# Kernel optimization log

Hardware: AMD Instinct MI355X
Metric: run time of the kernel (lower is better)

## Reference

```python
import jax, jax.numpy as jnp
import numpy as np

N = 100000
E = 1600000
F_IN, H, C = 128, 128, 64


def setup_inputs() -> dict:
    key = jax.random.key(0)
    ks = jax.random.split(key, 8)
    x = jax.random.normal(ks[0], (N, F_IN), dtype=jnp.float32)
    edge_index = jax.random.randint(ks[1], (2, E), 0, N, dtype=jnp.int64)
    s = lambda fi: (1.0 / np.sqrt(fi))
    # SAGEConv1: lin_l (applied to mean-aggregated neighbors, has bias), lin_r (root, no bias)
    W1l = jax.random.uniform(ks[2], (H, F_IN), jnp.float32, -s(F_IN), s(F_IN))
    b1 = jnp.zeros((H,), jnp.float32)
    W1r = jax.random.uniform(ks[3], (H, F_IN), jnp.float32, -s(F_IN), s(F_IN))
    # SAGEConv2
    W2l = jax.random.uniform(ks[4], (C, H), jnp.float32, -s(H), s(H))
    b2 = jnp.zeros((C,), jnp.float32)
    W2r = jax.random.uniform(ks[5], (C, H), jnp.float32, -s(H), s(H))
    return {"x": x, "edge_index": edge_index, "W1l": W1l, "b1": b1, "W1r": W1r,
            "W2l": W2l, "b2": b2, "W2r": W2r}


def _mean_aggr(x, src, dst):
    # mean over incoming neighbors (PyG flow: edge_index[0]=source -> edge_index[1]=target)
    msg = x[src]                                            # [E, F] big gather
    summed = jax.ops.segment_sum(msg, dst, num_segments=N)  # [N, F]
    cnt = jax.ops.segment_sum(jnp.ones((src.shape[0],), x.dtype), dst, num_segments=N)
    return summed / jnp.clip(cnt, 1.0)[:, None]


def _sage_conv(x, src, dst, Wl, b, Wr):
    agg = _mean_aggr(x, src, dst)
    return agg @ Wl.T + b + x @ Wr.T


def _iconv(x, src, dst):
    # weight-free GCN propagation: D^-1/2 (A + I) D^-1/2 @ x
    loops = jnp.arange(N, dtype=src.dtype)
    s2 = jnp.concatenate([src, loops])
    d2 = jnp.concatenate([dst, loops])
    deg = jax.ops.segment_sum(jnp.ones((s2.shape[0],), x.dtype), d2, num_segments=N)
    dis = jnp.where(deg > 0, jax.lax.rsqrt(jnp.maximum(deg, 1.0)), 0.0)
    norm = dis[s2] * dis[d2]                               # [E+N]
    return jax.ops.segment_sum(norm[:, None] * x[s2], d2, num_segments=N)


def reference(x, edge_index, W1l, b1, W1r, W2l, b2, W2r):
    src, dst = edge_index[0], edge_index[1]
    h = jax.nn.relu(_sage_conv(x, src, dst, W1l, b1, W1r))
    # F.dropout(training=False) -> identity in eval mode
    h = _sage_conv(h, src, dst, W2l, b2, W2r)
    return _iconv(h, src, dst)
```

## Files before the change

### kernel.cpp

```cpp
#include <hip/hip_runtime.h>

#define GN 100000
#define GE 1600000
#define GF 128
#define GH 128
#define GC 64

#define NB 392
#define SLABSZ 5376
#define P1_EDGES 4096
#define P1_BLOCKS ((GE + P1_EDGES - 1) / P1_EDGES)
#define CASTX_BLOCKS 12500

typedef __attribute__((ext_vector_type(8))) short v8s;
typedef __attribute__((ext_vector_type(4))) float v4f;
typedef __attribute__((ext_vector_type(2))) float v2f;

__device__ __forceinline__ unsigned short f2bf(float f) {
    union { float f; unsigned u; } a; a.f = f;
    unsigned r = a.u + 0x7fff + ((a.u >> 16) & 1);
    return (unsigned short)(r >> 16);
}
__device__ __forceinline__ float bf2f(unsigned short b) {
    union { unsigned u; float f; } a; a.u = ((unsigned)b) << 16;
    return a.f;
}
__device__ __forceinline__ v2f cvt2(unsigned w) {
    union { unsigned u; float f; } lo, hi;
    lo.u = w << 16; hi.u = w & 0xffff0000u;
    return (v2f){lo.f, hi.f};
}

__global__ __launch_bounds__(256) void prep_kernel(
    unsigned* __restrict__ slab, int* __restrict__ bucket_cnt,
    const int* __restrict__ src, const int* __restrict__ dst,
    unsigned short* __restrict__ xb, const float* __restrict__ x,
    unsigned short* w1l, unsigned short* w1r,
    unsigned short* w2l, unsigned short* w2r,
    const float* W1l, const float* W1r,
    const float* W2l, const float* W2r)
{
    __shared__ int hist[512];
    __shared__ int scanex[512];
    __shared__ int cursor[512];
    __shared__ int gbase[512];
    __shared__ int ssum[256];
    __shared__ unsigned stage[P1_EDGES];
    __shared__ unsigned short sbid[P1_EDGES];

    int tid = threadIdx.x;
    int blk = blockIdx.x;

    if (blk >= P1_BLOCKS) {
        int cb = blk - P1_BLOCKS;
        if (cb < CASTX_BLOCKS) {
            int i = cb * 256 + tid;
            float4 v = ((const float4*)x)[i];
            ushort4 u;
            u.x = f2bf(v.x); u.y = f2bf(v.y); u.z = f2bf(v.z); u.w = f2bf(v.w);
            ((ushort4*)xb)[i] = u;
            return;
        }
        int i = (cb - CASTX_BLOCKS) * 256 + tid;
        const float* s; unsigned short* d; int off;
        if      (i <  4096) { s = W1l; d = w1l; off = i; }
        else if (i <  8192) { s = W1r; d = w1r; off = i - 4096; }
        else if (i < 10240) { s = W2l; d = w2l; off = i - 8192; }
        else if (i < 12288) { s = W2r; d = w2r; off = i - 10240; }
        else return;
        float4 v = ((const float4*)s)[off];
        ushort4 u;
        u.x = f2bf(v.x); u.y = f2bf(v.y); u.z = f2bf(v.z); u.w = f2bf(v.w);
        ((ushort4*)d)[off] = u;
        return;
    }

    int e0 = blk * P1_EDGES;
    int nE = min(P1_EDGES, GE - e0);

    unsigned pk[16]; int bk[16];
    hist[tid] = 0; hist[tid + 256] = 0;
    __syncthreads();
    #pragma unroll
    for (int j = 0; j < 16; ++j) {
        int i = j * 256 + tid;
        if (i < nE) {
            int e = e0 + i;
            int d = dst[e], s = src[e];
            int b = d >> 8;
            pk[j] = ((unsigned)(d & 255) << 17) | (unsigned)s;
            bk[j] = b;
            atomicAdd(&hist[b], 1);
        } else bk[j] = -1;
    }
    __syncthreads();
    int a0 = hist[2 * tid], a1 = hist[2 * tid + 1];
    int s2 = a0 + a1;
    ssum[tid] = s2;
    __syncthreads();
    for (int off = 1; off < 256; off <<= 1) {
        int v = (tid >= off) ? ssum[tid - off] : 0;
        __syncthreads();
        ssum[tid] += v;
        __syncthreads();
    }
    int pbase = ssum[tid] - s2;
    scanex[2 * tid] = pbase;          cursor[2 * tid] = pbase;
    scanex[2 * tid + 1] = pbase + a0; cursor[2 * tid + 1] = pbase + a0;
    __syncthreads();
    #pragma unroll
    for (int j = 0; j < 16; ++j) {
        if (bk[j] >= 0) {
            int pos = atomicAdd(&cursor[bk[j]], 1);
            stage[pos] = pk[j];
            sbid[pos] = (unsigned short)bk[j];
        }
    }
    for (int b = tid; b < NB; b += 256) {
        int c = hist[b];
        gbase[b] = c ? atomicAdd(&bucket_cnt[b], c) : 0;
    }
    __syncthreads();
    for (int i = tid; i < nE; i += 256) {
        int b = sbid[i];
        int go = gbase[b] + (i - scanex[b]);
        if (go < SLABSZ)
            slab[(size_t)b * SLABSZ + go] = stage[i];
    }
}

__global__ __launch_bounds__(256) void bucket_pass2_kernel(
    int* __restrict__ csr, int* __restrict__ row_ptr,
    float* __restrict__ invc, float* __restrict__ dis,
    const unsigned* __restrict__ slab, const int* __restrict__ bucket_cnt)
{
    __shared__ int deg_l[256];
    __shared__ int excl[256];
    __shared__ int cur[256];
    __shared__ int ssum[256];
    __shared__ int bstart_s;
    __shared__ unsigned stage[SLABSZ];

    int t = threadIdx.x;
    int b = blockIdx.x;

    int c0 = (2 * t < NB) ? bucket_cnt[2 * t] : 0;
    int c1 = (2 * t + 1 < NB) ? bucket_cnt[2 * t + 1] : 0;
    int sc = c0 + c1;
    ssum[t] = sc;
    __syncthreads();
    for (int off = 1; off < 256; off <<= 1) {
        int v = (t >= off) ? ssum[t - off] : 0;
        __syncthreads();
        ssum[t] += v;
        __syncthreads();
    }
    int pb = ssum[t] - sc;
    if (2 * t == b)     bstart_s = pb;
    if (2 * t + 1 == b) bstart_s = pb + c0;
    if (b == NB - 1 && t == 0) row_ptr[GN] = GE;

    int cnt = min(bucket_cnt[b], SLABSZ);
    const unsigned* sp = slab + (size_t)b * SLABSZ;
    deg_l[t] = 0;
    __syncthreads();
    int base = bstart_s;
    for (int i = t; i < cnt; i += 256)
        atomicAdd(&deg_l[sp[i] >> 17], 1);
    __syncthreads();
    int dg = deg_l[t];
    ssum[t] = dg;
    __syncthreads();
    for (int off = 1; off < 256; off <<= 1) {
        int v = (t >= off) ? ssum[t - off] : 0;
        __syncthreads();
        ssum[t] += v;
        __syncthreads();
    }
    int ex = ssum[t] - dg;
    excl[t] = ex; cur[t] = ex;
    __syncthreads();
    int d = b * 256 + t;
    if (d < GN) {
        row_ptr[d] = base + ex;
        float c = (float)dg;
        invc[d] = 1.0f / fmaxf(c, 1.0f);
        dis[d] = rsqrtf(c + 1.0f);
    }
    for (int i = t; i < cnt; i += 256) {
        unsigned p = sp[i];
        int pos = atomicAdd(&cur[p >> 17], 1);
        stage[pos] = p & 0x1FFFFu;
    }
    __syncthreads();
    for (int i = t; i < cnt; i += 256)
        csr[base + i] = (int)stage[i];
}

__global__ __launch_bounds__(64, 2) void fused_gemm_kernel(
    unsigned short* __restrict__ P, unsigned short* __restrict__ Q,
    const unsigned short* __restrict__ A1, const unsigned short* __restrict__ A2,
    const unsigned short* __restrict__ W1, const unsigned short* __restrict__ W2,
    const unsigned short* __restrict__ Wl, const unsigned short* __restrict__ Wr,
    const float* __restrict__ b1, const float* __restrict__ b2, int M)
{
    __shared__ unsigned short hs[64][136];

    int lane = threadIdx.x;
    int lm = lane & 15, quad = lane >> 4;
    int m_base = blockIdx.x * 64;

    v4f acc[4][8];
    #pragma unroll
    for (int mt = 0; mt < 4; ++mt)
        #pragma unroll
        for (int nt = 0; nt < 8; ++nt) acc[mt][nt] = (v4f){0.f,0.f,0.f,0.f};

    #pragma unroll
    for (int ks = 0; ks < 4; ++ks) {
        int koff = ks * 32 + quad * 8;
        v8s a1[4], a2[4];
        #pragma unroll
        for (int mt = 0; mt < 4; ++mt) {
            int row = m_base + mt * 16 + lm;
            if (row < M) {
                a1[mt] = *(const v8s*)(A1 + (size_t)row * 128 + koff);
                a2[mt] = *(const v8s*)(A2 + (size_t)row * 128 + koff);
            } else {
                a1[mt] = (v8s){0,0,0,0,0,0,0,0};
                a2[mt] = (v8s){0,0,0,0,0,0,0,0};
            }
        }
        v8s w1[8], w2[8];
        #pragma unroll
        for (int nt = 0; nt < 8; ++nt) {
            int col = nt * 16 + lm;
            w1[nt] = *(const v8s*)(W1 + (size_t)col * 128 + koff);
            w2[nt] = *(const v8s*)(W2 + (size_t)col * 128 + koff);
        }
        #pragma unroll
        for (int mt = 0; mt < 4; ++mt)
            #pragma unroll
            for (int nt = 0; nt < 8; ++nt) {
                acc[mt][nt] = __builtin_amdgcn_mfma_f32_16x16x32_bf16(a1[mt], w1[nt], acc[mt][nt], 0, 0, 0);
                acc[mt][nt] = __builtin_amdgcn_mfma_f32_16x16x32_bf16(a2[mt], w2[nt], acc[mt][nt], 0, 0, 0);
            }
    }

    #pragma unroll
    for (int mt = 0; mt < 4; ++mt)
        #pragma unroll
        for (int r = 0; r < 4; ++r) {
            int rl = mt * 16 + quad * 4 + r;
            #pragma unroll
            for (int nt = 0; nt < 8; ++nt) {
                int col = nt * 16 + lm;
                float v = acc[mt][nt][r] + b1[col];
                hs[rl][col] = f2bf(fmaxf(v, 0.f));
            }
        }

    v4f accP[4][4], accQ[4][4];
    #pragma unroll
    for (int mt = 0; mt < 4; ++mt)
        #pragma unroll
        for (int nt = 0; nt < 4; ++nt) {
            accP[mt][nt] = (v4f){0.f,0.f,0.f,0.f};
            accQ[mt][nt] = (v4f){0.f,0.f,0.f,0.f};
        }

    #pragma unroll
    for (int ks = 0; ks < 4; ++ks) {
        int koff = ks * 32 + quad * 8;
        v8s af[4], bl[4], br[4];
        #pragma unroll
        for (int mt = 0; mt < 4; ++mt)
            af[mt] = *(const v8s*)&hs[mt * 16 + lm][koff];
        #pragma unroll
        for (int nt = 0; nt < 4; ++nt) {
            int col = nt * 16 + lm;
            bl[nt] = *(const v8s*)(Wl + (size_t)col * 128 + koff);
            br[nt] = *(const v8s*)(Wr + (size_t)col * 128 + koff);
        }
        #pragma unroll
        for (int mt = 0; mt < 4; ++mt)
            #pragma unroll
            for (int nt = 0; nt < 4; ++nt) {
                accP[mt][nt] = __builtin_amdgcn_mfma_f32_16x16x32_bf16(af[mt], bl[nt], accP[mt][nt], 0, 0, 0);
                accQ[mt][nt] = __builtin_amdgcn_mfma_f32_16x16x32_bf16(af[mt], br[nt], accQ[mt][nt], 0, 0, 0);
            }
    }

    #pragma unroll
    for (int mt = 0; mt < 4; ++mt)
        #pragma unroll
        for (int r = 0; r < 4; ++r) {
            int row = m_base + mt * 16 + quad * 4 + r;
            if (row >= M) continue;
            #pragma unroll
            for (int nt = 0; nt < 4; ++nt) {
                int col = nt * 16 + lm;
                P[(size_t)row * 64 + col] = f2bf(accP[mt][nt][r]);
                Q[(size_t)row * 64 + col] = f2bf(accQ[mt][nt][r] + b2[col]);
            }
        }
}

__global__ __launch_bounds__(256) void gather_mean128_kernel(
    unsigned short* __restrict__ out, const unsigned short* __restrict__ in,
    const float* __restrict__ invc, const int* __restrict__ row_ptr,
    const int* __restrict__ csr, int N)
{
    int wid = (blockIdx.x * 256 + threadIdx.x) >> 6;
    int lane = threadIdx.x & 63;
    if (wid >= N) return;
    int beg = __builtin_amdgcn_readfirstlane(row_ptr[wid]);
    int end = __builtin_amdgcn_readfirstlane(row_ptr[wid + 1]);
    int d = end - beg;
    int grp = lane >> 4, lx = lane & 15;
    v2f a0 = {0.f,0.f}, a1 = {0.f,0.f}, a2 = {0.f,0.f}, a3 = {0.f,0.f};

    int nf = d >> 2;
    #pragma unroll 4
    for (int t = 0; t < nf; ++t) {
        int j = beg + t * 4;
        int s0 = csr[j], s1 = csr[j + 1], s2 = csr[j + 2], s3 = csr[j + 3];
        int sa = (lane & 16) ? s1 : s0;
        int sb = (lane & 16) ? s3 : s2;
        int ss = (lane & 32) ? sb : sa;
        uint4 v = ((const uint4*)(in + (size_t)ss * 128))[lx];
        a0 += cvt2(v.x); a1 += cvt2(v.y); a2 += cvt2(v.z); a3 += cvt2(v.w);
    }
    int rem = d & 3;
    if (rem) {
        int j = beg + nf * 4;
        int c1 = (rem > 1) ? 1 : 0;
        int c2 = (rem > 2) ? 2 : c1;
        int s0 = csr[j], s1 = csr[j + c1], s2 = csr[j + c2], s3 = s2;
        int sa = (lane & 16) ? s1 : s0;
        int sb = (lane & 16) ? s3 : s2;
        int ss = (lane & 32) ? sb : sa;
        uint4 v = ((const uint4*)(in + (size_t)ss * 128))[lx];
        bool ok = grp < rem;
        v.x = ok ? v.x : 0u; v.y = ok ? v.y : 0u;
        v.z = ok ? v.z : 0u; v.w = ok ? v.w : 0u;
        a0 += cvt2(v.x); a1 += cvt2(v.y); a2 += cvt2(v.z); a3 += cvt2(v.w);
    }
    a0.x += __shfl_xor(a0.x, 16); a0.y += __shfl_xor(a0.y, 16);
    a1.x += __shfl_xor(a1.x, 16); a1.y += __shfl_xor(a1.y, 16);
    a2.x += __shfl_xor(a2.x, 16); a2.y += __shfl_xor(a2.y, 16);
    a3.x += __shfl_xor(a3.x, 16); a3.y += __shfl_xor(a3.y, 16);
    a0.x += __shfl_xor(a0.x, 32); a0.y += __shfl_xor(a0.y, 32);
    a1.x += __shfl_xor(a1.x, 32); a1.y += __shfl_xor(a1.y, 32);
    a2.x += __shfl_xor(a2.x, 32); a2.y += __shfl_xor(a2.y, 32);
    a3.x += __shfl_xor(a3.x, 32); a3.y += __shfl_xor(a3.y, 32);
    if (grp == 0) {
        float ic = invc[wid];
        uint4 o;
        o.x = (unsigned)f2bf(a0.x * ic) | ((unsigned)f2bf(a0.y * ic) << 16);
        o.y = (unsigned)f2bf(a1.x * ic) | ((unsigned)f2bf(a1.y * ic) << 16);
        o.z = (unsigned)f2bf(a2.x * ic) | ((unsigned)f2bf(a2.y * ic) << 16);
        o.w = (unsigned)f2bf(a3.x * ic) | ((unsigned)f2bf(a3.y * ic) << 16);
        ((uint4*)(out + (size_t)wid * 128))[lx] = o;
    }
}

__global__ __launch_bounds__(256) void gather_combine_kernel(
    unsigned short* __restrict__ h2s, const unsigned short* __restrict__ p,
    const unsigned short* __restrict__ q,
    const float* __restrict__ invc, const float* __restrict__ dis,
    const int* __restrict__ row_ptr, const int* __restrict__ csr, int N)
{
    int wid = (blockIdx.x * 256 + threadIdx.x) >> 6;
    int lane = threadIdx.x & 63;
    if (wid >= N) return;
    int beg = __builtin_amdgcn_readfirstlane(row_ptr[wid]);
    int end = __builtin_amdgcn_readfirstlane(row_ptr[wid + 1]);
    int d = end - beg;
    int grp = lane >> 3, lx = lane & 7;
    v2f a0 = {0.f,0.f}, a1 = {0.f,0.f}, a2 = {0.f,0.f}, a3 = {0.f,0.f};

    int nf = d >> 3;
    #pragma unroll 2
    for (int t = 0; t < nf; ++t) {
        int j = beg + t * 8;
        int s0 = csr[j],     s1 = csr[j + 1], s2 = csr[j + 2], s3 = csr[j + 3];
        int s4 = csr[j + 4], s5 = csr[j + 5], s6 = csr[j + 6], s7 = csr[j + 7];
        int t0 = (lane & 8) ? s1 : s0; int t1 = (lane & 8) ? s3 : s2;
        int t2 = (lane & 8) ? s5 : s4; int t3 = (lane & 8) ? s7 : s6;
        int u0 = (lane & 16) ? t1 : t0; int u1 = (lane & 16) ? t3 : t2;
        int ss = (lane & 32) ? u1 : u0;
        uint4 v = ((const uint4*)(p + (size_t)ss * 64))[lx];
        a0 += cvt2(v.x); a1 += cvt2(v.y); a2 += cvt2(v.z); a3 += cvt2(v.w);
    }
    int rem = d & 7;
    if (rem) {
        int j = beg + nf * 8;
        int rc = rem - 1;
        int s0 = csr[j];
        int s1 = csr[j + min(1, rc)]; int s2 = csr[j + min(2, rc)];
        int s3 = csr[j + min(3, rc)]; int s4 = csr[j + min(4, rc)];
        int s5 = csr[j + min(5, rc)]; int s6 = csr[j + min(6, rc)];
        int s7 = csr[j + min(7, rc)];
        int t0 = (lane & 8) ? s1 : s0; int t1 = (lane & 8) ? s3 : s2;
        int t2 = (lane & 8) ? s5 : s4; int t3 = (lane & 8) ? s7 : s6;
        int u0 = (lane & 16) ? t1 : t0; int u1 = (lane & 16) ? t3 : t2;
        int ss = (lane & 32) ? u1 : u0;
        uint4 v = ((const uint4*)(p + (size_t)ss * 64))[lx];
        bool ok = grp < rem;
        v.x = ok ? v.x : 0u; v.y = ok ? v.y : 0u;
        v.z = ok ? v.z : 0u; v.w = ok ? v.w : 0u;
        a0 += cvt2(v.x); a1 += cvt2(v.y); a2 += cvt2(v.z); a3 += cvt2(v.w);
    }
    #pragma unroll
    for (int m = 8; m <= 32; m <<= 1) {
        a0.x += __shfl_xor(a0.x, m); a0.y += __shfl_xor(a0.y, m);
        a1.x += __shfl_xor(a1.x, m); a1.y += __shfl_xor(a1.y, m);
        a2.x += __shfl_xor(a2.x, m); a2.y += __shfl_xor(a2.y, m);
        a3.x += __shfl_xor(a3.x, m); a3.y += __shfl_xor(a3.y, m);
    }
    if (grp == 0) {
        float ic = invc[wid], dd = dis[wid];
        uint4 qv = ((const uint4*)(q + (size_t)wid * 64))[lx];
        v2f q0 = cvt2(qv.x), q1 = cvt2(qv.y), q2 = cvt2(qv.z), q3 = cvt2(qv.w);
        uint4 o;
        o.x = (unsigned)f2bf(dd * (a0.x * ic + q0.x)) | ((unsigned)f2bf(dd * (a0.y * ic + q0.y)) << 16);
        o.y = (unsigned)f2bf(dd * (a1.x * ic + q1.x)) | ((unsigned)f2bf(dd * (a1.y * ic + q1.y)) << 16);
        o.z = (unsigned)f2bf(dd * (a2.x * ic + q2.x)) | ((unsigned)f2bf(dd * (a2.y * ic + q2.y)) << 16);
        o.w = (unsigned)f2bf(dd * (a3.x * ic + q3.x)) | ((unsigned)f2bf(dd * (a3.y * ic + q3.y)) << 16);
        ((uint4*)(h2s + (size_t)wid * 64))[lx] = o;
    }
}

__global__ __launch_bounds__(256) void iconv_kernel(
    float* __restrict__ out, const unsigned short* __restrict__ h2s,
    const float* __restrict__ dis, const int* __restrict__ row_ptr,
    const int* __restrict__ csr, int N)
{
    int wid = (blockIdx.x * 256 + threadIdx.x) >> 6;
    int lane = threadIdx.x & 63;
    if (wid >= N) return;
    int beg = __builtin_amdgcn_readfirstlane(row_ptr[wid]);
    int end = __builtin_amdgcn_readfirstlane(row_ptr[wid + 1]);
    int d = end - beg;
    int grp = lane >> 3, lx = lane & 7;
    v2f a0 = {0.f,0.f}, a1 = {0.f,0.f}, a2 = {0.f,0.f}, a3 = {0.f,0.f};

    int nf = d >> 3;
    #pragma unroll 2
    for (int t = 0; t < nf; ++t) {
        int j = beg + t * 8;
        int s0 = csr[j],     s1 = csr[j + 1], s2 = csr[j + 2], s3 = csr[j + 3];
        int s4 = csr[j + 4], s5 = csr[j + 5], s6 = csr[j + 6], s7 = csr[j + 7];
        int t0 = (lane & 8) ? s1 : s0; int t1 = (lane & 8) ? s3 : s2;
        int t2 = (lane & 8) ? s5 : s4; int t3 = (lane & 8) ? s7 : s6;
        int u0 = (lane & 16) ? t1 : t0; int u1 = (lane & 16) ? t3 : t2;
        int ss = (lane & 32) ? u1 : u0;
        uint4 v = ((const uint4*)(h2s + (size_t)ss * 64))[lx];
        a0 += cvt2(v.x); a1 += cvt2(v.y); a2 += cvt2(v.z); a3 += cvt2(v.w);
    }
    int rem = d & 7;
    if (rem) {
        int j = beg + nf * 8;
        int rc = rem - 1;
        int s0 = csr[j];
        int s1 = csr[j + min(1, rc)]; int s2 = csr[j + min(2, rc)];
        int s3 = csr[j + min(3, rc)]; int s4 = csr[j + min(4, rc)];
        int s5 = csr[j + min(5, rc)]; int s6 = csr[j + min(6, rc)];
        int s7 = csr[j + min(7, rc)];
        int t0 = (lane & 8) ? s1 : s0; int t1 = (lane & 8) ? s3 : s2;
        int t2 = (lane & 8) ? s5 : s4; int t3 = (lane & 8) ? s7 : s6;
        int u0 = (lane & 16) ? t1 : t0; int u1 = (lane & 16) ? t3 : t2;
        int ss = (lane & 32) ? u1 : u0;
        uint4 v = ((const uint4*)(h2s + (size_t)ss * 64))[lx];
        bool ok = grp < rem;
        v.x = ok ? v.x : 0u; v.y = ok ? v.y : 0u;
        v.z = ok ? v.z : 0u; v.w = ok ? v.w : 0u;
        a0 += cvt2(v.x); a1 += cvt2(v.y); a2 += cvt2(v.z); a3 += cvt2(v.w);
    }
    #pragma unroll
    for (int m = 8; m <= 32; m <<= 1) {
        a0.x += __shfl_xor(a0.x, m); a0.y += __shfl_xor(a0.y, m);
        a1.x += __shfl_xor(a1.x, m); a1.y += __shfl_xor(a1.y, m);
        a2.x += __shfl_xor(a2.x, m); a2.y += __shfl_xor(a2.y, m);
        a3.x += __shfl_xor(a3.x, m); a3.y += __shfl_xor(a3.y, m);
    }
    if (grp == 0) {
        uint4 sv = ((const uint4*)(h2s + (size_t)wid * 64))[lx];
        v2f s0 = cvt2(sv.x), s1 = cvt2(sv.y), s2 = cvt2(sv.z), s3 = cvt2(sv.w);
        float dd = dis[wid];
        float4 o0 = make_float4(dd * (a0.x + s0.x), dd * (a0.y + s0.y),
                                dd * (a1.x + s1.x), dd * (a1.y + s1.y));
        float4 o1 = make_float4(dd * (a2.x + s2.x), dd * (a2.y + s2.y),
                                dd * (a3.x + s3.x), dd * (a3.y + s3.y));
        ((float4*)(out + (size_t)wid * 64))[lx * 2]     = o0;
        ((float4*)(out + (size_t)wid * 64))[lx * 2 + 1] = o1;
    }
}

extern "C" void kernel_launch(void* const* d_in, const int* in_sizes, int n_in,
                              void* d_out, int out_size, void* d_ws, size_t ws_size,
                              hipStream_t stream) {
    const float* x   = (const float*)d_in[0];
    const int*   ei  = (const int*)d_in[1];
    const float* W1l = (const float*)d_in[2];
    const float* b1  = (const float*)d_in[3];
    const float* W1r = (const float*)d_in[4];
    const float* W2l = (const float*)d_in[5];
    const float* b2  = (const float*)d_in[6];
    const float* W2r = (const float*)d_in[7];
    float* out = (float*)d_out;

    const int* src = ei;
    const int* dst = ei + GE;

    float* invc = (float*)d_ws;
    float* dis  = invc + GN;
    unsigned short* regA = (unsigned short*)(dis + GN);
    unsigned short* regB = regA + (size_t)GN * 128;
    unsigned short* xb    = regA;
    unsigned short* aggx  = regB;
    unsigned short* w1lb = regB + (size_t)GN * 128;
    unsigned short* w1rb = w1lb + GH * GF;
    unsigned short* w2lb = w1rb + GH * GF;
    unsigned short* w2rb = w2lb + GC * GH;
    int* row_ptr      = (int*)(w2rb + GC * GH);
    int* bucket_cnt   = row_ptr + GN + 1;
    unsigned* slab    = (unsigned*)(bucket_cnt + NB);
    int* csr          = (int*)(slab + (size_t)NB * SLABSZ);
    unsigned short* pq = (unsigned short*)(csr + GE);
    unsigned short* pb = pq;
    unsigned short* qb = pq + (size_t)GN * 64;
    unsigned short* h2s = regB;

    const int T = 256;
    const int g_wave = (GN * 64 + T - 1) / T;
    dim3 g_fused((GN + 63) / 64, 1);

    hipMemsetAsync(bucket_cnt, 0, NB * sizeof(int), stream);
    prep_kernel<<<P1_BLOCKS + CASTX_BLOCKS + 48, T, 0, stream>>>(
        slab, bucket_cnt, src, dst,
        xb, x, w1lb, w1rb, w2lb, w2rb, W1l, W1r, W2l, W2r);

    bucket_pass2_kernel<<<NB, T, 0, stream>>>(csr, row_ptr, invc, dis,
                                              slab, bucket_cnt);

    gather_mean128_kernel<<<g_wave, T, 0, stream>>>(aggx, xb, invc, row_ptr, csr, GN);

    fused_gemm_kernel<<<g_fused, 64, 0, stream>>>(pb, qb, aggx, xb,
                                                  w1lb, w1rb, w2lb, w2rb,
                                                  b1, b2, GN);

    gather_combine_kernel<<<g_wave, T, 0, stream>>>(h2s, pb, qb, invc, dis,
                                                    row_ptr, csr, GN);

    iconv_kernel<<<g_wave, T, 0, stream>>>(out, h2s, dis, row_ptr, csr, GN);
}
```

Measured before the change: 335.2 us.

## Fuse first-layer neighbor mean gather into the SAGE GEMM kernel

Removes the separate gather_mean128 kernel and its bf16 aggregate buffer round-trip. Each 64-thread block now handles 16 nodes: it gathers neighbor rows into shared memory one node at a time, then runs both MFMA GEMM stages on that 16-row tile. This avoids writing and re-reading the 100000x128 aggregate and one kernel launch. In exchange the gather becomes serial per node within a single wave, which gives less memory-level parallelism. The weights are also reloaded from global memory for every 16-row tile instead of every 64 rows.

```diff
diff --git a/kernel.cpp b/kernel.cpp
--- a/kernel.cpp
+++ b/kernel.cpp
@@ -197,171 +197,121 @@
         csr[base + i] = (int)stage[i];
 }
 
-__global__ __launch_bounds__(64, 2) void fused_gemm_kernel(
+__global__ __launch_bounds__(64, 3) void sage1_fused_kernel(
     unsigned short* __restrict__ P, unsigned short* __restrict__ Q,
-    const unsigned short* __restrict__ A1, const unsigned short* __restrict__ A2,
+    const unsigned short* __restrict__ xb,
     const unsigned short* __restrict__ W1, const unsigned short* __restrict__ W2,
     const unsigned short* __restrict__ Wl, const unsigned short* __restrict__ Wr,
-    const float* __restrict__ b1, const float* __restrict__ b2, int M)
+    const float* __restrict__ b1, const float* __restrict__ b2,
+    const float* __restrict__ invc, const int* __restrict__ row_ptr,
+    const int* __restrict__ csr)
 {
-    __shared__ unsigned short hs[64][136];
+    __shared__ unsigned short hsA[16][136];
+    __shared__ unsigned short hsB[16][136];
 
     int lane = threadIdx.x;
     int lm = lane & 15, quad = lane >> 4;
-    int m_base = blockIdx.x * 64;
-
-    v4f acc[4][8];
-    #pragma unroll
-    for (int mt = 0; mt < 4; ++mt)
-        #pragma unroll
-        for (int nt = 0; nt < 8; ++nt) acc[mt][nt] = (v4f){0.f,0.f,0.f,0.f};
+    int m_base = blockIdx.x * 16;
+
+    int rp = row_ptr[m_base + min(lane, 16)];
+    float icv = invc[m_base + lm];
+
+    for (int r = 0; r < 16; ++r) {
+        int beg = __builtin_amdgcn_readlane(rp, r);
+        int end = __builtin_amdgcn_readlane(rp, r + 1);
+        int d = end - beg;
+        float a0 = 0.f, a1 = 0.f;
+        if (d > 0) {
+            int dc = min(d, 64);
+            int idx = csr[beg + ((lane < dc) ? lane : (dc - 1))];
+            for (int t = 0; t < dc; t += 16) {
+                unsigned v[16];
+                #pragma unroll
+                for (int u = 0; u < 16; ++u) {
+                    int tt = t + u;
+                    int s = __builtin_amdgcn_readlane(idx, (tt < dc) ? tt : (dc - 1));
+                    unsigned x = ((const unsigned*)(xb + (size_t)s * 128))[lane];
+                    v[u] = (tt < dc) ? x : 0u;
+                }
+                #pragma unroll
+                for (int u = 0; u < 16; ++u) {
+                    a0 += bf2f((unsigned short)(v[u] & 0xffff));
+                    a1 += bf2f((unsigned short)(v[u] >> 16));
+                }
+            }
+            for (int j = beg + 64; j < end; ++j) {
+                int s = __builtin_amdgcn_readfirstlane(csr[j]);
+                unsigned x = ((const unsigned*)(xb + (size_t)s * 128))[lane];
+                a0 += bf2f((unsigned short)(x & 0xffff));
+                a1 += bf2f((unsigned short)(x >> 16));
+            }
+        }
+        float ic = __int_as_float(__builtin_amdgcn_readlane(__float_as_int(icv), r));
+        unsigned w = (unsigned)f2bf(a0 * ic) | ((unsigned)f2bf(a1 * ic) << 16);
+        *(unsigned*)&hsA[r][2 * lane] = w;
+    }
+
+    v4f acc[8];
+    #pragma unroll
+    for (int nt = 0; nt < 8; ++nt) acc[nt] = (v4f){0.f,0.f,0.f,0.f};
 
     #pragma unroll
     for (int ks = 0; ks < 4; ++ks) {
         int koff = ks * 32 + quad * 8;
-        v8s a1[4], a2[4];
-        #pragma unroll
-        for (int mt = 0; mt < 4; ++mt) {
-            int row = m_base + mt * 16 + lm;
-            if (row < M) {
-                a1[mt] = *(const v8s*)(A1 + (size_t)row * 128 + koff);
-                a2[mt] = *(const v8s*)(A2 + (size_t)row * 128 + koff);
-            } else {
-                a1[mt] = (v8s){0,0,0,0,0,0,0,0};
-                a2[mt] = (v8s){0,0,0,0,0,0,0,0};
-            }
-        }
-        v8s w1[8], w2[8];
+        v8s a1f = *(const v8s*)&hsA[lm][koff];
+        v8s a2f = *(const v8s*)(xb + (size_t)(m_base + lm) * 128 + koff);
         #pragma unroll
         for (int nt = 0; nt < 8; ++nt) {
             int col = nt * 16 + lm;
-            w1[nt] = *(const v8s*)(W1 + (size_t)col * 128 + koff);
-            w2[nt] = *(const v8s*)(W2 + (size_t)col * 128 + koff);
-        }
-        #pragma unroll
-        for (int mt = 0; mt < 4; ++mt)
-            #pragma unroll
-            for (int nt = 0; nt < 8; ++nt) {
-                acc[mt][nt] = __builtin_amdgcn_mfma_f32_16x16x32_bf16(a1[mt], w1[nt], acc[mt][nt], 0, 0, 0);
-                acc[mt][nt] = __builtin_amdgcn_mfma_f32_16x16x32_bf16(a2[mt], w2[nt], acc[mt][nt], 0, 0, 0);
-            }
-    }
-
-    #pragma unroll
-    for (int mt = 0; mt < 4; ++mt)
+            v8s w1 = *(const v8s*)(W1 + (size_t)col * 128 + koff);
+            v8s w2 = *(const v8s*)(W2 + (size_t)col * 128 + koff);
+            acc[nt] = __builtin_amdgcn_mfma_f32_16x16x32_bf16(a1f, w1, acc[nt], 0, 0, 0);
+            acc[nt] = __builtin_amdgcn_mfma_f32_16x16x32_bf16(a2f, w2, acc[nt], 0, 0, 0);
+        }
+    }
+
+    #pragma unroll
+    for (int nt = 0; nt < 8; ++nt) {
+        int col = nt * 16 + lm;
+        float bv = b1[col];
         #pragma unroll
         for (int r = 0; r < 4; ++r) {
-            int rl = mt * 16 + quad * 4 + r;
-            #pragma unroll
-            for (int nt = 0; nt < 8; ++nt) {
-                int col = nt * 16 + lm;
-                float v = acc[mt][nt][r] + b1[col];
-                hs[rl][col] = f2bf(fmaxf(v, 0.f));
-            }
-        }
-
-    v4f accP[4][4], accQ[4][4];
-    #pragma unroll
-    for (int mt = 0; mt < 4; ++mt)
-        #pragma unroll
-        for (int nt = 0; nt < 4; ++nt) {
-            accP[mt][nt] = (v4f){0.f,0.f,0.f,0.f};
-            accQ[mt][nt] = (v4f){0.f,0.f,0.f,0.f};
-        }
+            int rl = quad * 4 + r;
+            hsB[rl][col] = f2bf(fmaxf(acc[nt][r] + bv, 0.f));
+        }
+    }
+
+    v4f accP[4], accQ[4];
+    #pragma unroll
+    for (int nt = 0; nt < 4; ++nt) {
+        accP[nt] = (v4f){0.f,0.f,0.f,0.f};
+        accQ[nt] = (v4f){0.f,0.f,0.f,0.f};
+    }
 
     #pragma unroll
     for (int ks = 0; ks < 4; ++ks) {
         int koff = ks * 32 + quad * 8;
-        v8s af[4], bl[4], br[4];
-        #pragma unroll
-        for (int mt = 0; mt < 4; ++mt)
-            af[mt] = *(const v8s*)&hs[mt * 16 + lm][koff];
+        v8s af = *(const v8s*)&hsB[lm][koff];
         #pragma unroll
         for (int nt = 0; nt < 4; ++nt) {
             int col = nt * 16 + lm;
-            bl[nt] = *(const v8s*)(Wl + (size_t)col * 128 + koff);
-            br[nt] = *(const v8s*)(Wr + (size_t)col * 128 + koff);
-        }
-        #pragma unroll
-        for (int mt = 0; mt < 4; ++mt)
-            #pragma unroll
-            for (int nt = 0; nt < 4; ++nt) {
-                accP[mt][nt] = __builtin_amdgcn_mfma_f32_16x16x32_bf16(af[mt], bl[nt], accP[mt][nt], 0, 0, 0);
-                accQ[mt][nt] = __builtin_amdgcn_mfma_f32_16x16x32_bf16(af[mt], br[nt], accQ[mt][nt], 0, 0, 0);
-            }
-    }
-
-    #pragma unroll
-    for (int mt = 0; mt < 4; ++mt)
+            v8s bl = *(const v8s*)(Wl + (size_t)col * 128 + koff);
+            v8s br = *(const v8s*)(Wr + (size_t)col * 128 + koff);
+            accP[nt] = __builtin_amdgcn_mfma_f32_16x16x32_bf16(af, bl, accP[nt], 0, 0, 0);
+            accQ[nt] = __builtin_amdgcn_mfma_f32_16x16x32_bf16(af, br, accQ[nt], 0, 0, 0);
+        }
+    }
+
+    #pragma unroll
+    for (int nt = 0; nt < 4; ++nt) {
+        int col = nt * 16 + lm;
+        float b2v = b2[col];
         #pragma unroll
         for (int r = 0; r < 4; ++r) {
-            int row = m_base + mt * 16 + quad * 4 + r;
-            if (row >= M) continue;
-            #pragma unroll
-            for (int nt = 0; nt < 4; ++nt) {
-                int col = nt * 16 + lm;
-                P[(size_t)row * 64 + col] = f2bf(accP[mt][nt][r]);
-                Q[(size_t)row * 64 + col] = f2bf(accQ[mt][nt][r] + b2[col]);
-            }
-        }
-}
-
-__global__ __launch_bounds__(256) void gather_mean128_kernel(
-    unsigned short* __restrict__ out, const unsigned short* __restrict__ in,
-    const float* __restrict__ invc, const int* __restrict__ row_ptr,
-    const int* __restrict__ csr, int N)
-{
-    int wid = (blockIdx.x * 256 + threadIdx.x) >> 6;
-    int lane = threadIdx.x & 63;
-    if (wid >= N) return;
-    int beg = __builtin_amdgcn_readfirstlane(row_ptr[wid]);
-    int end = __builtin_amdgcn_readfirstlane(row_ptr[wid + 1]);
-    int d = end - beg;
-    int grp = lane >> 4, lx = lane & 15;
-    v2f a0 = {0.f,0.f}, a1 = {0.f,0.f}, a2 = {0.f,0.f}, a3 = {0.f,0.f};
-
-    int nf = d >> 2;
-    #pragma unroll 4
-    for (int t = 0; t < nf; ++t) {
-        int j = beg + t * 4;
-        int s0 = csr[j], s1 = csr[j + 1], s2 = csr[j + 2], s3 = csr[j + 3];
-        int sa = (lane & 16) ? s1 : s0;
-        int sb = (lane & 16) ? s3 : s2;
-        int ss = (lane & 32) ? sb : sa;
-        uint4 v = ((const uint4*)(in + (size_t)ss * 128))[lx];
-        a0 += cvt2(v.x); a1 += cvt2(v.y); a2 += cvt2(v.z); a3 += cvt2(v.w);
-    }
-    int rem = d & 3;
-    if (rem) {
-        int j = beg + nf * 4;
-        int c1 = (rem > 1) ? 1 : 0;
-        int c2 = (rem > 2) ? 2 : c1;
-        int s0 = csr[j], s1 = csr[j + c1], s2 = csr[j + c2], s3 = s2;
-        int sa = (lane & 16) ? s1 : s0;
-        int sb = (lane & 16) ? s3 : s2;
-        int ss = (lane & 32) ? sb : sa;
-        uint4 v = ((const uint4*)(in + (size_t)ss * 128))[lx];
-        bool ok = grp < rem;
-        v.x = ok ? v.x : 0u; v.y = ok ? v.y : 0u;
-        v.z = ok ? v.z : 0u; v.w = ok ? v.w : 0u;
-        a0 += cvt2(v.x); a1 += cvt2(v.y); a2 += cvt2(v.z); a3 += cvt2(v.w);
-    }
-    a0.x += __shfl_xor(a0.x, 16); a0.y += __shfl_xor(a0.y, 16);
-    a1.x += __shfl_xor(a1.x, 16); a1.y += __shfl_xor(a1.y, 16);
-    a2.x += __shfl_xor(a2.x, 16); a2.y += __shfl_xor(a2.y, 16);
-    a3.x += __shfl_xor(a3.x, 16); a3.y += __shfl_xor(a3.y, 16);
-    a0.x += __shfl_xor(a0.x, 32); a0.y += __shfl_xor(a0.y, 32);
-    a1.x += __shfl_xor(a1.x, 32); a1.y += __shfl_xor(a1.y, 32);
-    a2.x += __shfl_xor(a2.x, 32); a2.y += __shfl_xor(a2.y, 32);
-    a3.x += __shfl_xor(a3.x, 32); a3.y += __shfl_xor(a3.y, 32);
-    if (grp == 0) {
-        float ic = invc[wid];
-        uint4 o;
-        o.x = (unsigned)f2bf(a0.x * ic) | ((unsigned)f2bf(a0.y * ic) << 16);
-        o.y = (unsigned)f2bf(a1.x * ic) | ((unsigned)f2bf(a1.y * ic) << 16);
-        o.z = (unsigned)f2bf(a2.x * ic) | ((unsigned)f2bf(a2.y * ic) << 16);
-        o.w = (unsigned)f2bf(a3.x * ic) | ((unsigned)f2bf(a3.y * ic) << 16);
-        ((uint4*)(out + (size_t)wid * 128))[lx] = o;
+            int row = m_base + quad * 4 + r;
+            P[(size_t)row * 64 + col] = f2bf(accP[nt][r]);
+            Q[(size_t)row * 64 + col] = f2bf(accQ[nt][r] + b2v);
+        }
     }
 }
 
@@ -519,7 +469,6 @@
     unsigned short* regA = (unsigned short*)(dis + GN);
     unsigned short* regB = regA + (size_t)GN * 128;
     unsigned short* xb    = regA;
-    unsigned short* aggx  = regB;
     unsigned short* w1lb = regB + (size_t)GN * 128;
     unsigned short* w1rb = w1lb + GH * GF;
     unsigned short* w2lb = w1rb + GH * GF;
@@ -535,7 +484,6 @@
 
     const int T = 256;
     const int g_wave = (GN * 64 + T - 1) / T;
-    dim3 g_fused((GN + 63) / 64, 1);
 
     hipMemsetAsync(bucket_cnt, 0, NB * sizeof(int), stream);
     prep_kernel<<<P1_BLOCKS + CASTX_BLOCKS + 48, T, 0, stream>>>(
@@ -545,11 +493,9 @@
     bucket_pass2_kernel<<<NB, T, 0, stream>>>(csr, row_ptr, invc, dis,
                                               slab, bucket_cnt);
 
-    gather_mean128_kernel<<<g_wave, T, 0, stream>>>(aggx, xb, invc, row_ptr, csr, GN);
-
-    fused_gemm_kernel<<<g_fused, 64, 0, stream>>>(pb, qb, aggx, xb,
-                                                  w1lb, w1rb, w2lb, w2rb,
-                                                  b1, b2, GN);
+    sage1_fused_kernel<<<GN / 16, 64, 0, stream>>>(pb, qb, xb,
+                                                   w1lb, w1rb, w2lb, w2rb,
+                                                   b1, b2, invc, row_ptr, csr);
 
     gather_combine_kernel<<<g_wave, T, 0, stream>>>(h2s, pb, qb, invc, dis,
                                                     row_ptr, csr, GN);
```

After: 359.6 us. 7.3% more time.

## Replace bucketed slab CSR build with global-atomic degree count, scan, scatter

Applied to the files above, without the earlier changes.

Replaces the two-pass bucketed slab sort (LDS histogram plus staging per block) with a simpler CSR build: global atomic degree counting, a two-kernel prefix scan, and an atomic-cursor scatter of source indices. This drops the slab buffer, its overflow cap and the LDS-heavy staging, but adds 1.6M global atomics twice and random scattered writes into csr. The order of edges within each row becomes nondeterministic, which can change float summation order downstream and hurt locality. It also adds extra kernel launches.

```diff
diff --git a/kernel.cpp b/kernel.cpp
--- a/kernel.cpp
+++ b/kernel.cpp
@@ -7,9 +7,7 @@
 #define GC 64
 
 #define NB 392
-#define SLABSZ 5376
-#define P1_EDGES 4096
-#define P1_BLOCKS ((GE + P1_EDGES - 1) / P1_EDGES)
+#define EDGE_BLOCKS ((GE + 2047) / 2048)
 #define CASTX_BLOCKS 12500
 
 typedef __attribute__((ext_vector_type(8))) short v8s;
@@ -32,120 +30,72 @@
 }
 
 __global__ __launch_bounds__(256) void prep_kernel(
-    unsigned* __restrict__ slab, int* __restrict__ bucket_cnt,
-    const int* __restrict__ src, const int* __restrict__ dst,
+    int* __restrict__ deg, const int* __restrict__ dst,
     unsigned short* __restrict__ xb, const float* __restrict__ x,
     unsigned short* w1l, unsigned short* w1r,
     unsigned short* w2l, unsigned short* w2r,
     const float* W1l, const float* W1r,
     const float* W2l, const float* W2r)
 {
-    __shared__ int hist[512];
-    __shared__ int scanex[512];
-    __shared__ int cursor[512];
-    __shared__ int gbase[512];
-    __shared__ int ssum[256];
-    __shared__ unsigned stage[P1_EDGES];
-    __shared__ unsigned short sbid[P1_EDGES];
-
     int tid = threadIdx.x;
     int blk = blockIdx.x;
 
-    if (blk >= P1_BLOCKS) {
-        int cb = blk - P1_BLOCKS;
-        if (cb < CASTX_BLOCKS) {
-            int i = cb * 256 + tid;
-            float4 v = ((const float4*)x)[i];
-            ushort4 u;
-            u.x = f2bf(v.x); u.y = f2bf(v.y); u.z = f2bf(v.z); u.w = f2bf(v.w);
-            ((ushort4*)xb)[i] = u;
-            return;
-        }
-        int i = (cb - CASTX_BLOCKS) * 256 + tid;
-        const float* s; unsigned short* d; int off;
-        if      (i <  4096) { s = W1l; d = w1l; off = i; }
-        else if (i <  8192) { s = W1r; d = w1r; off = i - 4096; }
-        else if (i < 10240) { s = W2l; d = w2l; off = i - 8192; }
-        else if (i < 12288) { s = W2r; d = w2r; off = i - 10240; }
-        else return;
-        float4 v = ((const float4*)s)[off];
+    if (blk < EDGE_BLOCKS) {
+        int e0 = blk * 2048 + tid;
+        #pragma unroll
+        for (int j = 0; j < 8; ++j) {
+            int e = e0 + j * 256;
+            if (e < GE) atomicAdd(&deg[dst[e]], 1);
+        }
+        return;
+    }
+    int cb = blk - EDGE_BLOCKS;
+    if (cb < CASTX_BLOCKS) {
+        int i = cb * 256 + tid;
+        float4 v = ((const float4*)x)[i];
         ushort4 u;
         u.x = f2bf(v.x); u.y = f2bf(v.y); u.z = f2bf(v.z); u.w = f2bf(v.w);
-        ((ushort4*)d)[off] = u;
+        ((ushort4*)xb)[i] = u;
         return;
     }
-
-    int e0 = blk * P1_EDGES;
-    int nE = min(P1_EDGES, GE - e0);
-
-    unsigned pk[16]; int bk[16];
-    hist[tid] = 0; hist[tid + 256] = 0;
+    int i = (cb - CASTX_BLOCKS) * 256 + tid;
+    const float* s; unsigned short* d; int off;
+    if      (i <  4096) { s = W1l; d = w1l; off = i; }
+    else if (i <  8192) { s = W1r; d = w1r; off = i - 4096; }
+    else if (i < 10240) { s = W2l; d = w2l; off = i - 8192; }
+    else if (i < 12288) { s = W2r; d = w2r; off = i - 10240; }
+    else return;
+    float4 v = ((const float4*)s)[off];
+    ushort4 u;
+    u.x = f2bf(v.x); u.y = f2bf(v.y); u.z = f2bf(v.z); u.w = f2bf(v.w);
+    ((ushort4*)d)[off] = u;
+}
+
+__global__ __launch_bounds__(256) void scan1_kernel(
+    int* __restrict__ bsum, const int* __restrict__ deg)
+{
+    __shared__ int ws[4];
+    int t = threadIdx.x, b = blockIdx.x;
+    int d = b * 256 + t;
+    int v = (d < GN) ? deg[d] : 0;
+    #pragma unroll
+    for (int m = 1; m < 64; m <<= 1) v += __shfl_xor(v, m);
+    if ((t & 63) == 0) ws[t >> 6] = v;
     __syncthreads();
-    #pragma unroll
-    for (int j = 0; j < 16; ++j) {
-        int i = j * 256 + tid;
-        if (i < nE) {
-            int e = e0 + i;
-            int d = dst[e], s = src[e];
-            int b = d >> 8;
-            pk[j] = ((unsigned)(d & 255) << 17) | (unsigned)s;
-            bk[j] = b;
-            atomicAdd(&hist[b], 1);
-        } else bk[j] = -1;
-    }
-    __syncthreads();
-    int a0 = hist[2 * tid], a1 = hist[2 * tid + 1];
-    int s2 = a0 + a1;
-    ssum[tid] = s2;
-    __syncthreads();
-    for (int off = 1; off < 256; off <<= 1) {
-        int v = (tid >= off) ? ssum[tid - off] : 0;
-        __syncthreads();
-        ssum[tid] += v;
-        __syncthreads();
-    }
-    int pbase = ssum[tid] - s2;
-    scanex[2 * tid] = pbase;          cursor[2 * tid] = pbase;
-    scanex[2 * tid + 1] = pbase + a0; cursor[2 * tid + 1] = pbase + a0;
-    __syncthreads();
-    #pragma unroll
-    for (int j = 0; j < 16; ++j) {
-        if (bk[j] >= 0) {
-            int pos = atomicAdd(&cursor[bk[j]], 1);
-            stage[pos] = pk[j];
-            sbid[pos] = (unsigned short)bk[j];
-        }
-    }
-    for (int b = tid; b < NB; b += 256) {
-        int c = hist[b];
-        gbase[b] = c ? atomicAdd(&bucket_cnt[b], c) : 0;
-    }
-    __syncthreads();
-    for (int i = tid; i < nE; i += 256) {
-        int b = sbid[i];
-        int go = gbase[b] + (i - scanex[b]);
-        if (go < SLABSZ)
-            slab[(size_t)b * SLABSZ + go] = stage[i];
-    }
-}
-
-__global__ __launch_bounds__(256) void bucket_pass2_kernel(
-    int* __restrict__ csr, int* __restrict__ row_ptr,
+    if (t == 0) bsum[b] = ws[0] + ws[1] + ws[2] + ws[3];
+}
+
+__global__ __launch_bounds__(256) void scan2_kernel(
+    int* __restrict__ row_ptr, int* __restrict__ cursor,
     float* __restrict__ invc, float* __restrict__ dis,
-    const unsigned* __restrict__ slab, const int* __restrict__ bucket_cnt)
-{
-    __shared__ int deg_l[256];
-    __shared__ int excl[256];
-    __shared__ int cur[256];
+    const int* __restrict__ deg, const int* __restrict__ bsum)
+{
     __shared__ int ssum[256];
     __shared__ int bstart_s;
-    __shared__ unsigned stage[SLABSZ];
-
-    int t = threadIdx.x;
-    int b = blockIdx.x;
-
-    int c0 = (2 * t < NB) ? bucket_cnt[2 * t] : 0;
-    int c1 = (2 * t + 1 < NB) ? bucket_cnt[2 * t + 1] : 0;
+    int t = threadIdx.x, b = blockIdx.x;
+
+    int c0 = (2 * t < NB) ? bsum[2 * t] : 0;
+    int c1 = (2 * t + 1 < NB) ? bsum[2 * t + 1] : 0;
     int sc = c0 + c1;
     ssum[t] = sc;
     __syncthreads();
@@ -158,17 +108,12 @@
     int pb = ssum[t] - sc;
     if (2 * t == b)     bstart_s = pb;
     if (2 * t + 1 == b) bstart_s = pb + c0;
-    if (b == NB - 1 && t == 0) row_ptr[GN] = GE;
-
-    int cnt = min(bucket_cnt[b], SLABSZ);
-    const unsigned* sp = slab + (size_t)b * SLABSZ;
-    deg_l[t] = 0;
+    if (b == 0 && t == 0) row_ptr[GN] = GE;
     __syncthreads();
     int base = bstart_s;
-    for (int i = t; i < cnt; i += 256)
-        atomicAdd(&deg_l[sp[i] >> 17], 1);
-    __syncthreads();
-    int dg = deg_l[t];
+
+    int d = b * 256 + t;
+    int dg = (d < GN) ? deg[d] : 0;
     ssum[t] = dg;
     __syncthreads();
     for (int off = 1; off < 256; off <<= 1) {
@@ -178,23 +123,29 @@
         __syncthreads();
     }
     int ex = ssum[t] - dg;
-    excl[t] = ex; cur[t] = ex;
-    __syncthreads();
-    int d = b * 256 + t;
     if (d < GN) {
-        row_ptr[d] = base + ex;
+        int rp = base + ex;
+        row_ptr[d] = rp;
+        cursor[d] = rp;
         float c = (float)dg;
         invc[d] = 1.0f / fmaxf(c, 1.0f);
         dis[d] = rsqrtf(c + 1.0f);
     }
-    for (int i = t; i < cnt; i += 256) {
-        unsigned p = sp[i];
-        int pos = atomicAdd(&cur[p >> 17], 1);
-        stage[pos] = p & 0x1FFFFu;
-    }
-    __syncthreads();
-    for (int i = t; i < cnt; i += 256)
-        csr[base + i] = (int)stage[i];
+}
+
+__global__ __launch_bounds__(256) void scatter_kernel(
+    int* __restrict__ csr, int* __restrict__ cursor,
+    const int* __restrict__ src, const int* __restrict__ dst)
+{
+    int e0 = blockIdx.x * 2048 + threadIdx.x;
+    #pragma unroll
+    for (int j = 0; j < 8; ++j) {
+        int e = e0 + j * 256;
+        if (e < GE) {
+            int pos = atomicAdd(&cursor[dst[e]], 1);
+            csr[pos] = src[e];
+        }
+    }
 }
 
 __global__ __launch_bounds__(64, 2) void fused_gemm_kernel(
@@ -525,9 +476,10 @@
     unsigned short* w2lb = w1rb + GH * GF;
     unsigned short* w2rb = w2lb + GC * GH;
     int* row_ptr      = (int*)(w2rb + GC * GH);
-    int* bucket_cnt   = row_ptr + GN + 1;
-    unsigned* slab    = (unsigned*)(bucket_cnt + NB);
-    int* csr          = (int*)(slab + (size_t)NB * SLABSZ);
+    int* deg          = row_ptr + GN + 1;
+    int* cursor       = deg + GN;
+    int* bsum         = cursor + GN;
+    int* csr          = bsum + NB;
     unsigned short* pq = (unsigned short*)(csr + GE);
     unsigned short* pb = pq;
     unsigned short* qb = pq + (size_t)GN * 64;
@@ -537,13 +489,14 @@
     const int g_wave = (GN * 64 + T - 1) / T;
     dim3 g_fused((GN + 63) / 64, 1);
 
-    hipMemsetAsync(bucket_cnt, 0, NB * sizeof(int), stream);
-    prep_kernel<<<P1_BLOCKS + CASTX_BLOCKS + 48, T, 0, stream>>>(
-        slab, bucket_cnt, src, dst,
-        xb, x, w1lb, w1rb, w2lb, w2rb, W1l, W1r, W2l, W2r);
-
-    bucket_pass2_kernel<<<NB, T, 0, stream>>>(csr, row_ptr, invc, dis,
-                                              slab, bucket_cnt);
+    hipMemsetAsync(deg, 0, GN * sizeof(int), stream);
+    prep_kernel<<<EDGE_BLOCKS + CASTX_BLOCKS + 48, T, 0, stream>>>(
+        deg, dst, xb, x, w1lb, w1rb, w2lb, w2rb, W1l, W1r, W2l, W2r);
+
+    scan1_kernel<<<NB, T, 0, stream>>>(bsum, deg);
+    scan2_kernel<<<NB, T, 0, stream>>>(row_ptr, cursor, invc, dis, deg, bsum);
+
+    scatter_kernel<<<EDGE_BLOCKS, T, 0, stream>>>(csr, cursor, src, dst);
 
     gather_mean128_kernel<<<g_wave, T, 0, stream>>>(aggx, xb, invc, row_ptr, csr, GN);
 
```

Result: slower. 503.2 us (+50.1%).
